# Performance work log

Measured on AMD Instinct MI355X. Metric: run time of the kernel, lower is better.

## Reference

```python
import jax, jax.numpy as jnp
import numpy as np

B, T, D, M = 128, 2048, 128, 64


def setup_inputs() -> dict:
    key = jax.random.key(0)
    ks = jax.random.split(key, 8)
    q = jax.random.normal(ks[0], (B, T, D), jnp.float32)
    qa = jax.random.normal(ks[1], (B, T, D), jnp.float32)
    MS = jax.random.normal(ks[2], (M, D), jnp.float32)
    # kaiming_normal_ init: std = sqrt(2 / fan_in)
    dy_mem = jax.random.normal(ks[3], (M, D), jnp.float32) * np.float32(np.sqrt(2.0 / D))
    lim = np.float32(1.0 / np.sqrt(D))  # torch nn.Linear default init
    e_w = jax.random.uniform(ks[4], (D, D), jnp.float32, -lim, lim)
    e_b = jax.random.uniform(ks[5], (D,), jnp.float32, -lim, lim)
    a_w = jax.random.uniform(ks[6], (D, D), jnp.float32, -lim, lim)
    a_b = jax.random.uniform(ks[7], (D,), jnp.float32, -lim, lim)
    return dict(q=q, qa=qa, MS=MS, dy_mem=dy_mem, e_w=e_w, e_b=e_b, a_w=a_w, a_b=a_b)


def reference(q, qa, MS, dy_mem, e_w, e_b, a_w, a_b):
    # q, qa: [B, T, D]; MS, dy_mem: [M, D]
    batch = q.shape[0]
    w = jax.nn.softmax(jnp.einsum('btd,md->btm', q, MS), axis=-1)  # [B,T,M]
    e = jax.nn.sigmoid(qa @ e_w.T + e_b)  # erase gate, [B,T,D]
    a = jnp.tanh(qa @ a_w.T + a_b)        # add gate,   [B,T,D]

    mem0 = jnp.broadcast_to(dy_mem, (batch,) + dy_mem.shape)  # [B,M,D]

    def step(mem, xs):
        wt, et, at = xs  # [B,M], [B,D], [B,D]
        # readout uses state BEFORE the write (final_mem[:, :-1] in the original)
        read = jnp.einsum('bm,bmd->bd', wt, mem)
        mem = mem * (1.0 - wt[:, :, None] * et[:, None, :]) + wt[:, :, None] * at[:, None, :]
        return mem, read

    _, reads = jax.lax.scan(
        step, mem0,
        (w.transpose(1, 0, 2), e.transpose(1, 0, 2), a.transpose(1, 0, 2)),
    )  # reads: [T,B,D]
    return reads.transpose(1, 0, 2)  # [B,T,D]
```

## Files before the change

kernel.cpp:

```cpp
#include <hip/hip_runtime.h>
#include <math.h>

#define B_  128
#define T_  2048
#define D_  128
#define M_  64
#define BT_ (B_*T_)
#define TC_ 64
#define NC_ (T_/TC_)

#define GLL16(src, dst)                                                     \
  __builtin_amdgcn_global_load_lds(                                         \
      (const __attribute__((address_space(1))) void*)(src),                 \
      (__attribute__((address_space(3))) void*)(dst), 16, 0, 0)

__global__ void k_transpose(const float* __restrict__ e_w,
                            const float* __restrict__ a_w,
                            const float* __restrict__ MS,
                            float* __restrict__ Wt) {
  int k = blockIdx.x;
  int n = threadIdx.x;
  float v;
  if (n < 128)      v = e_w[n * D_ + k];
  else if (n < 256) v = a_w[(n - 128) * D_ + k];
  else              v = MS[(n - 256) * D_ + k];
  Wt[k * 320 + n] = v;
}

__global__ __launch_bounds__(256, 2)
void k_gemm(const float* __restrict__ q, const float* __restrict__ qa,
            const float* __restrict__ Wt, const float* __restrict__ e_b,
            const float* __restrict__ a_b, float* __restrict__ w_ws,
            float* __restrict__ e_ws, float* __restrict__ a_ws) {
  __shared__ float Wl[128 * 64];
  __shared__ float Xl[2][128 * 32];

  const int nb  = blockIdx.x;
  const int rb  = blockIdx.y;
  const int tid = threadIdx.x;
  const int tx  = tid & 15;
  const int ty  = tid >> 4;
  const int r0  = rb * 128;
  const int n0  = nb * 64;
  const float* X = (nb == 4) ? q : qa;

#pragma unroll
  for (int i = 0; i < 8; ++i) {
    int u = tid + i * 256;
    int k = u >> 4, col = (u & 15) * 4;
    GLL16(Wt + (size_t)k * 320 + n0 + col, Wl + u * 4);
  }

  auto STAGEX = [&](int buf, int k0) {
#pragma unroll
    for (int i = 0; i < 4; ++i) {
      int u   = tid + i * 256;
      int row = u >> 3;
      int kb  = u & 7;
      int kbs = (kb + (row >> 3)) & 7;
      GLL16(X + (size_t)(r0 + row) * 128 + k0 + kbs * 4, Xl[buf] + u * 4);
    }
  };

  float acc[8][4];
#pragma unroll
  for (int i = 0; i < 8; ++i)
#pragma unroll
    for (int j = 0; j < 4; ++j) acc[i][j] = 0.f;

  STAGEX(0, 0);
  __syncthreads();

  const int rot = ty & 7;
  for (int c = 0; c < 4; ++c) {
    if (c < 3) STAGEX((c + 1) & 1, (c + 1) * 32);
    const float* Xb = Xl[c & 1];
    const float* Wb = Wl + c * 32 * 64;
#pragma unroll
    for (int k4 = 0; k4 < 8; ++k4) {
      float4 wv[4];
#pragma unroll
      for (int kk = 0; kk < 4; ++kk)
        wv[kk] = *(const float4*)(Wb + (size_t)(k4 * 4 + kk) * 64 + tx * 4);
      const int ldsb = (k4 - rot) & 7;
#pragma unroll
      for (int i = 0; i < 8; ++i) {
        float4 xv = *(const float4*)(Xb + (size_t)(ty * 8 + i) * 32 + ldsb * 4);
#pragma unroll
        for (int kk = 0; kk < 4; ++kk) {
          float xk = ((const float*)&xv)[kk];
          acc[i][0] = fmaf(xk, wv[kk].x, acc[i][0]);
          acc[i][1] = fmaf(xk, wv[kk].y, acc[i][1]);
          acc[i][2] = fmaf(xk, wv[kk].z, acc[i][2]);
          acc[i][3] = fmaf(xk, wv[kk].w, acc[i][3]);
        }
      }
    }
    __syncthreads();
  }

  if (nb == 4) {
#pragma unroll
    for (int i = 0; i < 8; ++i) {
      float mx = fmaxf(fmaxf(acc[i][0], acc[i][1]), fmaxf(acc[i][2], acc[i][3]));
#pragma unroll
      for (int s = 1; s < 16; s <<= 1) mx = fmaxf(mx, __shfl_xor(mx, s));
      float e0 = expf(acc[i][0] - mx);
      float e1 = expf(acc[i][1] - mx);
      float e2 = expf(acc[i][2] - mx);
      float e3 = expf(acc[i][3] - mx);
      float sum = e0 + e1 + e2 + e3;
#pragma unroll
      for (int s = 1; s < 16; s <<= 1) sum += __shfl_xor(sum, s);
      float inv = 1.0f / sum;
      float4 o = make_float4(e0 * inv, e1 * inv, e2 * inv, e3 * inv);
      *(float4*)(w_ws + (size_t)(r0 + ty * 8 + i) * M_ + tx * 4) = o;
    }
  } else {
    const int n = n0 + tx * 4;
    const bool is_e = (n < 128);
    const float* bias = is_e ? (e_b + n) : (a_b + (n - 128));
    float b0 = bias[0], b1 = bias[1], b2 = bias[2], b3 = bias[3];
    float* dst = is_e ? e_ws : a_ws;
    const int cn = n & 127;
#pragma unroll
    for (int i = 0; i < 8; ++i) {
      float x0 = acc[i][0] + b0, x1 = acc[i][1] + b1;
      float x2 = acc[i][2] + b2, x3 = acc[i][3] + b3;
      float4 o;
      if (is_e) {
        o.x = 1.f / (1.f + expf(-x0));
        o.y = 1.f / (1.f + expf(-x1));
        o.z = 1.f / (1.f + expf(-x2));
        o.w = 1.f / (1.f + expf(-x3));
      } else {
        o.x = tanhf(x0); o.y = tanhf(x1); o.z = tanhf(x2); o.w = tanhf(x3);
      }
      *(float4*)(dst + (size_t)(r0 + ty * 8 + i) * D_ + cn) = o;
    }
  }
}

__global__ __launch_bounds__(256, 1)
void k_scan(const float* __restrict__ w_ws, const float* __restrict__ e_ws,
            const float* __restrict__ a_ws, const float* __restrict__ dy,
            float* __restrict__ out) {
  __shared__ float lds[2][TC_ * 128];

  int o  = ((blockIdx.x & 7) << 6) | (blockIdx.x >> 3);
  int b  = o >> 2;
  int dq = o & 3;

  int tid  = threadIdx.x;
  int lane = tid & 63;
  int mg   = lane & 7;
  int dl   = ((tid >> 6) << 3) | (lane >> 3);
  int d    = (dq << 5) + dl;
  int m0   = mg << 3;

  float mem[8];
#pragma unroll
  for (int j = 0; j < 8; ++j) mem[j] = dy[(size_t)(m0 + j) * D_ + d];

  const float* wbase = w_ws + (size_t)b * T_ * M_;
  const float* ebase = e_ws + (size_t)b * T_ * D_ + dq * 32;
  const float* abase = a_ws + (size_t)b * T_ * D_ + dq * 32;
  float*       op    = out  + (size_t)b * T_ * D_ + d;

  auto STAGE = [&](int buf, int c) {
    int t0 = c * TC_;
    float* L = lds[buf];
#pragma unroll
    for (int i = 0; i < 4; ++i) {
      int u = tid + i * 256;
      GLL16(wbase + (size_t)t0 * 64 + u * 4, L + u * 4);
    }
#pragma unroll
    for (int i = 0; i < 2; ++i) {
      int u  = tid + i * 256;
      int tt = u >> 3, inner = (u & 7) * 4;
      GLL16(ebase + (size_t)(t0 + tt) * D_ + inner, L + TC_ * 64 + u * 4);
    }
#pragma unroll
    for (int i = 0; i < 2; ++i) {
      int u  = tid + i * 256;
      int tt = u >> 3, inner = (u & 7) * 4;
      GLL16(abase + (size_t)(t0 + tt) * D_ + inner, L + TC_ * 96 + u * 4);
    }
  };

  STAGE(0, 0);
  __syncthreads();

  for (int c = 0; c < NC_; ++c) {
    if (c + 1 < NC_) STAGE((c + 1) & 1, c + 1);
    const float* L  = lds[c & 1];
    const float* Lw = L;
    const float* Le = L + TC_ * 64;
    const float* La = L + TC_ * 96;
    const int t0 = c * TC_;
#pragma unroll 8
    for (int tt = 0; tt < TC_; ++tt) {
      float4 wlo = *(const float4*)(Lw + tt * 64 + m0);
      float4 whi = *(const float4*)(Lw + tt * 64 + m0 + 4);
      float  e   = Le[tt * 32 + dl];
      float  a   = La[tt * 32 + dl];
      float wvv[8] = {wlo.x, wlo.y, wlo.z, wlo.w, whi.x, whi.y, whi.z, whi.w};
      float r = 0.f;
#pragma unroll
      for (int j = 0; j < 8; ++j) {
        r = fmaf(wvv[j], mem[j], r);
        float h = fmaf(-e, mem[j], a);
        mem[j]  = fmaf(wvv[j], h, mem[j]);
      }
      r += __shfl_xor(r, 1);
      r += __shfl_xor(r, 2);
      r += __shfl_xor(r, 4);
      if (mg == 0) op[(size_t)(t0 + tt) * D_] = r;
    }
    __syncthreads();
  }
}

extern "C" void kernel_launch(void* const* d_in, const int* in_sizes, int n_in,
                              void* d_out, int out_size, void* d_ws, size_t ws_size,
                              hipStream_t stream) {
  const float* q      = (const float*)d_in[0];
  const float* qa     = (const float*)d_in[1];
  const float* MS     = (const float*)d_in[2];
  const float* dy_mem = (const float*)d_in[3];
  const float* e_w    = (const float*)d_in[4];
  const float* e_b    = (const float*)d_in[5];
  const float* a_w    = (const float*)d_in[6];
  const float* a_b    = (const float*)d_in[7];
  float* out = (float*)d_out;

  float* Wt  = (float*)d_ws;
  float* wws = Wt  + (size_t)128 * 320;
  float* ews = wws + (size_t)BT_ * M_;
  float* aws = ews + (size_t)BT_ * D_;

  k_transpose<<<128, 320, 0, stream>>>(e_w, a_w, MS, Wt);
  k_gemm<<<dim3(5, BT_ / 128), 256, 0, stream>>>(q, qa, Wt, e_b, a_b,
                                                 wws, ews, aws);
  k_scan<<<512, 256, 0, stream>>>(wws, ews, aws, dy_mem, out);
}
```

Baseline: 998.3 us.

## Enlarge per-thread tiles in GEMM and scan, add DPP reductions and XCD-aware mapping

```diff
diff --git a/kernel.cpp b/kernel.cpp
--- a/kernel.cpp
+++ b/kernel.cpp
@@ -13,6 +13,27 @@
   __builtin_amdgcn_global_load_lds(                                         \
       (const __attribute__((address_space(1))) void*)(src),                 \
       (__attribute__((address_space(3))) void*)(dst), 16, 0, 0)
+
+__device__ __forceinline__ float dpp_add8(float x) {
+  int v;
+  v = __builtin_amdgcn_update_dpp(0, __float_as_int(x), 0xB1, 0xf, 0xf, true);
+  x += __int_as_float(v);
+  v = __builtin_amdgcn_update_dpp(0, __float_as_int(x), 0x4E, 0xf, 0xf, true);
+  x += __int_as_float(v);
+  v = __builtin_amdgcn_update_dpp(0, __float_as_int(x), 0x141, 0xf, 0xf, true);
+  x += __int_as_float(v);
+  return x;
+}
+__device__ __forceinline__ float dpp_max8(float x) {
+  int v;
+  v = __builtin_amdgcn_update_dpp(0, __float_as_int(x), 0xB1, 0xf, 0xf, true);
+  x = fmaxf(x, __int_as_float(v));
+  v = __builtin_amdgcn_update_dpp(0, __float_as_int(x), 0x4E, 0xf, 0xf, true);
+  x = fmaxf(x, __int_as_float(v));
+  v = __builtin_amdgcn_update_dpp(0, __float_as_int(x), 0x141, 0xf, 0xf, true);
+  x = fmaxf(x, __int_as_float(v));
+  return x;
+}
 
 __global__ void k_transpose(const float* __restrict__ e_w,
                             const float* __restrict__ a_w,
@@ -27,7 +48,7 @@
   Wt[k * 320 + n] = v;
 }
 
-__global__ __launch_bounds__(256, 2)
+__global__ __launch_bounds__(128, 1)
 void k_gemm(const float* __restrict__ q, const float* __restrict__ qa,
             const float* __restrict__ Wt, const float* __restrict__ e_b,
             const float* __restrict__ a_b, float* __restrict__ w_ws,
@@ -35,26 +56,29 @@
   __shared__ float Wl[128 * 64];
   __shared__ float Xl[2][128 * 32];
 
-  const int nb  = blockIdx.x;
-  const int rb  = blockIdx.y;
-  const int tid = threadIdx.x;
-  const int tx  = tid & 15;
-  const int ty  = tid >> 4;
-  const int r0  = rb * 128;
-  const int n0  = nb * 64;
+  const int bid  = blockIdx.x;
+  const int xcd  = bid & 7;
+  const int i    = bid >> 3;
+  const int nb   = i % 5;
+  const int rb   = xcd * 256 + i / 5;
+  const int tid  = threadIdx.x;
+  const int tx   = tid & 7;
+  const int ty   = tid >> 3;
+  const int r0   = rb * 128;
+  const int n0   = nb * 64;
   const float* X = (nb == 4) ? q : qa;
 
 #pragma unroll
-  for (int i = 0; i < 8; ++i) {
-    int u = tid + i * 256;
+  for (int u16 = 0; u16 < 16; ++u16) {
+    int u = tid + u16 * 128;
     int k = u >> 4, col = (u & 15) * 4;
     GLL16(Wt + (size_t)k * 320 + n0 + col, Wl + u * 4);
   }
 
   auto STAGEX = [&](int buf, int k0) {
 #pragma unroll
-    for (int i = 0; i < 4; ++i) {
-      int u   = tid + i * 256;
+    for (int u8 = 0; u8 < 8; ++u8) {
+      int u   = tid + u8 * 128;
       int row = u >> 3;
       int kb  = u & 7;
       int kbs = (kb + (row >> 3)) & 7;
@@ -62,11 +86,11 @@
     }
   };
 
-  float acc[8][4];
-#pragma unroll
-  for (int i = 0; i < 8; ++i)
-#pragma unroll
-    for (int j = 0; j < 4; ++j) acc[i][j] = 0.f;
+  float acc[8][8];
+#pragma unroll
+  for (int a = 0; a < 8; ++a)
+#pragma unroll
+    for (int b = 0; b < 8; ++b) acc[a][b] = 0.f;
 
   STAGEX(0, 0);
   __syncthreads();
@@ -78,21 +102,30 @@
     const float* Wb = Wl + c * 32 * 64;
 #pragma unroll
     for (int k4 = 0; k4 < 8; ++k4) {
-      float4 wv[4];
-#pragma unroll
-      for (int kk = 0; kk < 4; ++kk)
-        wv[kk] = *(const float4*)(Wb + (size_t)(k4 * 4 + kk) * 64 + tx * 4);
       const int ldsb = (k4 - rot) & 7;
-#pragma unroll
-      for (int i = 0; i < 8; ++i) {
-        float4 xv = *(const float4*)(Xb + (size_t)(ty * 8 + i) * 32 + ldsb * 4);
-#pragma unroll
-        for (int kk = 0; kk < 4; ++kk) {
-          float xk = ((const float*)&xv)[kk];
-          acc[i][0] = fmaf(xk, wv[kk].x, acc[i][0]);
-          acc[i][1] = fmaf(xk, wv[kk].y, acc[i][1]);
-          acc[i][2] = fmaf(xk, wv[kk].z, acc[i][2]);
-          acc[i][3] = fmaf(xk, wv[kk].w, acc[i][3]);
+      float4 xv[8];
+#pragma unroll
+      for (int r = 0; r < 8; ++r)
+        xv[r] = *(const float4*)(Xb + (size_t)(ty * 8 + r) * 32 + ldsb * 4);
+      float4 wv0[4], wv1[4];
+#pragma unroll
+      for (int kk = 0; kk < 4; ++kk) {
+        wv0[kk] = *(const float4*)(Wb + (size_t)(k4 * 4 + kk) * 64 + tx * 8);
+        wv1[kk] = *(const float4*)(Wb + (size_t)(k4 * 4 + kk) * 64 + tx * 8 + 4);
+      }
+#pragma unroll
+      for (int kk = 0; kk < 4; ++kk) {
+#pragma unroll
+        for (int r = 0; r < 8; ++r) {
+          float xk = ((const float*)&xv[r])[kk];
+          acc[r][0] = fmaf(xk, wv0[kk].x, acc[r][0]);
+          acc[r][1] = fmaf(xk, wv0[kk].y, acc[r][1]);
+          acc[r][2] = fmaf(xk, wv0[kk].z, acc[r][2]);
+          acc[r][3] = fmaf(xk, wv0[kk].w, acc[r][3]);
+          acc[r][4] = fmaf(xk, wv1[kk].x, acc[r][4]);
+          acc[r][5] = fmaf(xk, wv1[kk].y, acc[r][5]);
+          acc[r][6] = fmaf(xk, wv1[kk].z, acc[r][6]);
+          acc[r][7] = fmaf(xk, wv1[kk].w, acc[r][7]);
         }
       }
     }
@@ -101,42 +134,44 @@
 
   if (nb == 4) {
 #pragma unroll
-    for (int i = 0; i < 8; ++i) {
-      float mx = fmaxf(fmaxf(acc[i][0], acc[i][1]), fmaxf(acc[i][2], acc[i][3]));
-#pragma unroll
-      for (int s = 1; s < 16; s <<= 1) mx = fmaxf(mx, __shfl_xor(mx, s));
-      float e0 = expf(acc[i][0] - mx);
-      float e1 = expf(acc[i][1] - mx);
-      float e2 = expf(acc[i][2] - mx);
-      float e3 = expf(acc[i][3] - mx);
-      float sum = e0 + e1 + e2 + e3;
-#pragma unroll
-      for (int s = 1; s < 16; s <<= 1) sum += __shfl_xor(sum, s);
+    for (int r = 0; r < 8; ++r) {
+      float mx = acc[r][0];
+#pragma unroll
+      for (int j = 1; j < 8; ++j) mx = fmaxf(mx, acc[r][j]);
+      mx = dpp_max8(mx);
+      float ex[8]; float sum = 0.f;
+#pragma unroll
+      for (int j = 0; j < 8; ++j) { ex[j] = expf(acc[r][j] - mx); sum += ex[j]; }
+      sum = dpp_add8(sum);
       float inv = 1.0f / sum;
-      float4 o = make_float4(e0 * inv, e1 * inv, e2 * inv, e3 * inv);
-      *(float4*)(w_ws + (size_t)(r0 + ty * 8 + i) * M_ + tx * 4) = o;
+      float* dst = w_ws + (size_t)(r0 + ty * 8 + r) * M_ + tx * 8;
+      *(float4*)(dst)     = make_float4(ex[0]*inv, ex[1]*inv, ex[2]*inv, ex[3]*inv);
+      *(float4*)(dst + 4) = make_float4(ex[4]*inv, ex[5]*inv, ex[6]*inv, ex[7]*inv);
     }
   } else {
-    const int n = n0 + tx * 4;
+    const int n = n0 + tx * 8;
     const bool is_e = (n < 128);
     const float* bias = is_e ? (e_b + n) : (a_b + (n - 128));
-    float b0 = bias[0], b1 = bias[1], b2 = bias[2], b3 = bias[3];
-    float* dst = is_e ? e_ws : a_ws;
+    float bb[8];
+#pragma unroll
+    for (int j = 0; j < 8; ++j) bb[j] = bias[j];
+    float* dst0 = is_e ? e_ws : a_ws;
     const int cn = n & 127;
 #pragma unroll
-    for (int i = 0; i < 8; ++i) {
-      float x0 = acc[i][0] + b0, x1 = acc[i][1] + b1;
-      float x2 = acc[i][2] + b2, x3 = acc[i][3] + b3;
-      float4 o;
+    for (int r = 0; r < 8; ++r) {
+      float o[8];
       if (is_e) {
-        o.x = 1.f / (1.f + expf(-x0));
-        o.y = 1.f / (1.f + expf(-x1));
-        o.z = 1.f / (1.f + expf(-x2));
-        o.w = 1.f / (1.f + expf(-x3));
+#pragma unroll
+        for (int j = 0; j < 8; ++j)
+          o[j] = 1.f / (1.f + expf(-(acc[r][j] + bb[j])));
       } else {
-        o.x = tanhf(x0); o.y = tanhf(x1); o.z = tanhf(x2); o.w = tanhf(x3);
-      }
-      *(float4*)(dst + (size_t)(r0 + ty * 8 + i) * D_ + cn) = o;
+#pragma unroll
+        for (int j = 0; j < 8; ++j)
+          o[j] = tanhf(acc[r][j] + bb[j]);
+      }
+      float* dst = dst0 + (size_t)(r0 + ty * 8 + r) * D_ + cn;
+      *(float4*)(dst)     = make_float4(o[0], o[1], o[2], o[3]);
+      *(float4*)(dst + 4) = make_float4(o[4], o[5], o[6], o[7]);
     }
   }
 }
@@ -145,47 +180,52 @@
 void k_scan(const float* __restrict__ w_ws, const float* __restrict__ e_ws,
             const float* __restrict__ a_ws, const float* __restrict__ dy,
             float* __restrict__ out) {
-  __shared__ float lds[2][TC_ * 128];
-
-  int o  = ((blockIdx.x & 7) << 6) | (blockIdx.x >> 3);
-  int b  = o >> 2;
-  int dq = o & 3;
-
-  int tid  = threadIdx.x;
-  int lane = tid & 63;
-  int mg   = lane & 7;
-  int dl   = ((tid >> 6) << 3) | (lane >> 3);
-  int d    = (dq << 5) + dl;
-  int m0   = mg << 3;
-
-  float mem[8];
-#pragma unroll
-  for (int j = 0; j < 8; ++j) mem[j] = dy[(size_t)(m0 + j) * D_ + d];
+  __shared__ float lds[2][TC_ * 192];
+
+  int o = ((blockIdx.x & 7) << 5) | (blockIdx.x >> 3);
+  int b = o >> 1;
+  int h = o & 1;
+
+  const int tid  = threadIdx.x;
+  const int lane = tid & 63;
+  const int wv   = tid >> 6;
+  const int mg   = lane & 7;
+  const int dl8  = lane >> 3;
+  const int m0   = mg << 3;
+  const int dloc = (wv << 4) + (dl8 << 1);
+  const int d    = (h << 6) + dloc;
+
+  float mem[8][2];
+#pragma unroll
+  for (int j = 0; j < 8; ++j) {
+    mem[j][0] = dy[(size_t)(m0 + j) * D_ + d];
+    mem[j][1] = dy[(size_t)(m0 + j) * D_ + d + 1];
+  }
 
   const float* wbase = w_ws + (size_t)b * T_ * M_;
-  const float* ebase = e_ws + (size_t)b * T_ * D_ + dq * 32;
-  const float* abase = a_ws + (size_t)b * T_ * D_ + dq * 32;
+  const float* ebase = e_ws + (size_t)b * T_ * D_ + (h << 6);
+  const float* abase = a_ws + (size_t)b * T_ * D_ + (h << 6);
   float*       op    = out  + (size_t)b * T_ * D_ + d;
 
   auto STAGE = [&](int buf, int c) {
-    int t0 = c * TC_;
+    const int t0 = c * TC_;
     float* L = lds[buf];
 #pragma unroll
-    for (int i = 0; i < 4; ++i) {
-      int u = tid + i * 256;
+    for (int u4 = 0; u4 < 4; ++u4) {
+      int u = tid + u4 * 256;
       GLL16(wbase + (size_t)t0 * 64 + u * 4, L + u * 4);
     }
 #pragma unroll
-    for (int i = 0; i < 2; ++i) {
-      int u  = tid + i * 256;
-      int tt = u >> 3, inner = (u & 7) * 4;
-      GLL16(ebase + (size_t)(t0 + tt) * D_ + inner, L + TC_ * 64 + u * 4);
-    }
-#pragma unroll
-    for (int i = 0; i < 2; ++i) {
-      int u  = tid + i * 256;
-      int tt = u >> 3, inner = (u & 7) * 4;
-      GLL16(abase + (size_t)(t0 + tt) * D_ + inner, L + TC_ * 96 + u * 4);
+    for (int u4 = 0; u4 < 4; ++u4) {
+      int u = tid + u4 * 256;
+      int t = u >> 4, inner = (u & 15) * 4;
+      GLL16(ebase + (size_t)(t0 + t) * D_ + inner, L + TC_ * 64 + u * 4);
+    }
+#pragma unroll
+    for (int u4 = 0; u4 < 4; ++u4) {
+      int u = tid + u4 * 256;
+      int t = u >> 4, inner = (u & 15) * 4;
+      GLL16(abase + (size_t)(t0 + t) * D_ + inner, L + TC_ * 128 + u * 4);
     }
   };
 
@@ -194,29 +234,41 @@
 
   for (int c = 0; c < NC_; ++c) {
     if (c + 1 < NC_) STAGE((c + 1) & 1, c + 1);
-    const float* L  = lds[c & 1];
-    const float* Lw = L;
-    const float* Le = L + TC_ * 64;
-    const float* La = L + TC_ * 96;
+    const float* Lw = lds[c & 1];
+    const float* Le = Lw + TC_ * 64;
+    const float* La = Lw + TC_ * 128;
     const int t0 = c * TC_;
-#pragma unroll 8
+
+    float4 nw0 = *(const float4*)(Lw + m0);
+    float4 nw1 = *(const float4*)(Lw + m0 + 4);
+    float2 ne  = *(const float2*)(Le + dloc);
+    float2 na  = *(const float2*)(La + dloc);
+
+#pragma unroll 4
     for (int tt = 0; tt < TC_; ++tt) {
-      float4 wlo = *(const float4*)(Lw + tt * 64 + m0);
-      float4 whi = *(const float4*)(Lw + tt * 64 + m0 + 4);
-      float  e   = Le[tt * 32 + dl];
-      float  a   = La[tt * 32 + dl];
-      float wvv[8] = {wlo.x, wlo.y, wlo.z, wlo.w, whi.x, whi.y, whi.z, whi.w};
-      float r = 0.f;
+      float4 w0 = nw0, w1 = nw1;
+      float2 ev = ne, av = na;
+      int tn = (tt + 1 < TC_) ? tt + 1 : TC_ - 1;
+      nw0 = *(const float4*)(Lw + tn * 64 + m0);
+      nw1 = *(const float4*)(Lw + tn * 64 + m0 + 4);
+      ne  = *(const float2*)(Le + tn * 64 + dloc);
+      na  = *(const float2*)(La + tn * 64 + dloc);
+
+      float wv8[8] = {w0.x, w0.y, w0.z, w0.w, w1.x, w1.y, w1.z, w1.w};
+      float r0 = 0.f, r1 = 0.f;
 #pragma unroll
       for (int j = 0; j < 8; ++j) {
-        r = fmaf(wvv[j], mem[j], r);
-        float h = fmaf(-e, mem[j], a);
-        mem[j]  = fmaf(wvv[j], h, mem[j]);
-      }
-      r += __shfl_xor(r, 1);
-      r += __shfl_xor(r, 2);
-      r += __shfl_xor(r, 4);
-      if (mg == 0) op[(size_t)(t0 + tt) * D_] = r;
+        r0 = fmaf(wv8[j], mem[j][0], r0);
+        r1 = fmaf(wv8[j], mem[j][1], r1);
+        float h0 = fmaf(-ev.x, mem[j][0], av.x);
+        float h1 = fmaf(-ev.y, mem[j][1], av.y);
+        mem[j][0] = fmaf(wv8[j], h0, mem[j][0]);
+        mem[j][1] = fmaf(wv8[j], h1, mem[j][1]);
+      }
+      r0 = dpp_add8(r0);
+      r1 = dpp_add8(r1);
+      if (mg == 0)
+        *(float2*)(op + (size_t)(t0 + tt) * D_) = make_float2(r0, r1);
     }
     __syncthreads();
   }
@@ -241,7 +293,6 @@
   float* aws = ews + (size_t)BT_ * D_;
 
   k_transpose<<<128, 320, 0, stream>>>(e_w, a_w, MS, Wt);
-  k_gemm<<<dim3(5, BT_ / 128), 256, 0, stream>>>(q, qa, Wt, e_b, a_b,
-                                                 wws, ews, aws);
-  k_scan<<<512, 256, 0, stream>>>(wws, ews, aws, dy_mem, out);
-}
+  k_gemm<<<10240, 128, 0, stream>>>(q, qa, Wt, e_b, a_b, wws, ews, aws);
+  k_scan<<<256, 256, 0, stream>>>(wws, ews, aws, dy_mem, out);
+}
```

Result: no change. 1.018 ms (+2.0%).
